# Performance work log

Hardware: AMD Instinct MI355X
Metric: run time of the kernel (lower is better)

## Reference

```python
import jax, jax.numpy as jnp
import numpy as np

T, B, H, O = 512, 64, 512, 128
G = 4 * H  # PyTorch gate order: i, f, g, o


def setup_inputs() -> dict:
    key = jax.random.key(0)
    ks = jax.random.split(key, 10)
    s = 1.0 / np.sqrt(H)
    return {
        "x": jax.random.normal(ks[0], (T, B, H), jnp.float32),
        "h0": jnp.zeros((1, B, H), jnp.float32),
        "c0": jnp.zeros((1, B, H), jnp.float32),
        "W_ih1": jax.random.normal(ks[1], (G, H), jnp.float32) * s,
        "W_hh1": jax.random.normal(ks[2], (G, H), jnp.float32) * s,
        "b_ih1": jax.random.normal(ks[3], (G,), jnp.float32) * s,
        "b_hh1": jax.random.normal(ks[4], (G,), jnp.float32) * s,
        "W_ih2": jax.random.normal(ks[5], (G, H), jnp.float32) * s,
        "W_hh2": jax.random.normal(ks[6], (G, H), jnp.float32) * s,
        "b_ih2": jax.random.normal(ks[7], (G,), jnp.float32) * s,
        "b_hh2": jax.random.normal(ks[8], (G,), jnp.float32) * s,
        "W_out": jax.random.normal(ks[9], (O, H), jnp.float32) * s,
        "b_out": jnp.zeros((O,), jnp.float32),
    }


def _lstm_layer(x, h0, c0, W_ih, W_hh, b_ih, b_hh):
    # x: [T,B,H]; h0,c0: [B,H]. PyTorch LSTM math, gate order i,f,g,o.
    xg = jnp.einsum('tbh,gh->tbg', x, W_ih) + b_ih + b_hh  # [T,B,4H]
    W_hh_T = W_hh.T

    def step(carry, xg_t):
        h, c = carry
        g = xg_t + h @ W_hh_T
        i, f, gc, o = jnp.split(g, 4, axis=-1)
        i = jax.nn.sigmoid(i)
        f = jax.nn.sigmoid(f)
        gc = jnp.tanh(gc)
        o = jax.nn.sigmoid(o)
        c = f * c + i * gc
        h = o * jnp.tanh(c)
        return (h, c), h

    (hT, cT), ys = jax.lax.scan(step, (h0, c0), xg)
    return ys, hT, cT


def reference(x, h0, c0, W_ih1, W_hh1, b_ih1, b_hh1, W_ih2, W_hh2, b_ih2, b_hh2, W_out, b_out):
    y1, h1, c1 = _lstm_layer(x, h0[0], c0[0], W_ih1, W_hh1, b_ih1, b_hh1)
    # Faithful quirk: lstm2 is initialized with lstm1's FINAL (h, c).
    y2, h2, c2 = _lstm_layer(y1, h1, c1, W_ih2, W_hh2, b_ih2, b_hh2)
    out = y2[-1] @ W_out.T + b_out  # Linear on last timestep; LogSoftmax is unused in forward
    return out, h2[None], c2[None]
```

## Files before the change

kernel.cpp:

```cpp
#include <hip/hip_runtime.h>

typedef unsigned short u16;
typedef unsigned int u32;
typedef unsigned long long u64;
using f32x4 = __attribute__((ext_vector_type(4))) float;
using s16x8 = __attribute__((ext_vector_type(8))) short;
using u64x2 = __attribute__((ext_vector_type(2))) unsigned long long;

constexpr int Tn = 512, Bn = 64, Hn = 512, Gn = 2048, On = 128;
constexpr int NS = 16;
constexpr int NG = 4;

constexpr size_t OFF_CMID = 0;
constexpr size_t OFF_HMID = OFF_CMID + (size_t)Bn * Hn * 4;
constexpr size_t OFF_XBF  = OFF_HMID + (size_t)Bn * Hn * 4;
constexpr size_t OFF_HT1  = OFF_XBF + (size_t)Tn * Bn * Hn * 2;
constexpr size_t OFF_HT2  = OFF_HT1 + (size_t)(Tn + 1) * Bn * Hn * 2;

__device__ __forceinline__ u16 f2b(float f) {
  union { float f; unsigned u; } v; v.f = f;
  unsigned r = v.u + 0x7fffu + ((v.u >> 16) & 1u);
  return (u16)(r >> 16);
}
__device__ __forceinline__ float b2f(u16 u) {
  union { unsigned u; float f; } v; v.u = ((unsigned)u) << 16; return v.f;
}
__device__ __forceinline__ s16x8 pack8(float4 lo, float4 hi) {
  s16x8 r;
  r[0] = (short)f2b(lo.x); r[1] = (short)f2b(lo.y); r[2] = (short)f2b(lo.z); r[3] = (short)f2b(lo.w);
  r[4] = (short)f2b(hi.x); r[5] = (short)f2b(hi.y); r[6] = (short)f2b(hi.z); r[7] = (short)f2b(hi.w);
  return r;
}
__device__ __forceinline__ float sigm(float x) {
  float e = __builtin_amdgcn_exp2f(-1.4426950408889634f * x);
  return __builtin_amdgcn_rcpf(1.0f + e);
}
__device__ __forceinline__ float tanh_(float x) {
  float e = __builtin_amdgcn_exp2f(-2.885390081777927f * x);
  return __builtin_amdgcn_rcpf(1.0f + e) * 2.0f - 1.0f;
}
__device__ __forceinline__ u64 ld64_sc(const u64* p) {
  return __hip_atomic_load(p, __ATOMIC_RELAXED, __HIP_MEMORY_SCOPE_AGENT);
}
__device__ __forceinline__ void st64_sc(u64* p, u64 v) {
  __hip_atomic_store(p, v, __ATOMIC_RELAXED, __HIP_MEMORY_SCOPE_AGENT);
}

__global__ __launch_bounds__(256)
void cvt_kernel(const float* __restrict__ in, u16* __restrict__ out, int n4) {
  const int i = blockIdx.x * 256 + threadIdx.x;
  if (i < n4) {
    float4 v = ((const float4*)in)[i];
    ushort4 o; o.x = f2b(v.x); o.y = f2b(v.y); o.z = f2b(v.z); o.w = f2b(v.w);
    ((ushort4*)out)[i] = o;
  }
}

__global__ __launch_bounds__(256, 1)
void scan_fused(const u16* __restrict__ xin, const float* __restrict__ Whh,
                const float* __restrict__ Wih, const float* __restrict__ bih,
                const float* __restrict__ bhh,
                const float* __restrict__ hinit, const float* __restrict__ cinit,
                u16* __restrict__ ht, float* __restrict__ h_fin, float* __restrict__ c_fin)
{
  const int g = blockIdx.x >> 4, s = blockIdx.x & (NS - 1);
  const int tid = threadIdx.x;
  const int lane = tid & 63, w = tid >> 6;
  const int x16 = lane & 15, grp = lane >> 4;
  const int jj = x16 & 7;
  const int j0 = s * 32 + w * 8;
  const int brow = g * 16;
  const int bth = brow + grp * 4;

  __shared__ char hlds[16 * 1024];
  __shared__ char xlds[2 * 16 * 1024];
  __shared__ u16 hstage[16][32];

  const size_t grow0 = (size_t)(0 * 2 + (x16 >> 3)) * Hn + j0 + jj;
  const size_t grow1 = (size_t)(2 + (x16 >> 3)) * Hn + j0 + jj;
  s16x8 bwh[2][16], bwi[2][16];
#pragma unroll
  for (int nt = 0; nt < 2; ++nt) {
    const size_t grow = nt ? grow1 : grow0;
#pragma unroll
    for (int ks = 0; ks < 16; ++ks) {
      const float* wp = Whh + grow * Hn + ks * 32 + grp * 8;
      float4 lo = *(const float4*)wp, hi = *(const float4*)(wp + 4);
      bwh[nt][ks] = pack8(lo, hi);
      const float* wq = Wih + grow * Hn + ks * 32 + grp * 8;
      float4 lo2 = *(const float4*)wq, hi2 = *(const float4*)(wq + 4);
      bwi[nt][ks] = pack8(lo2, hi2);
    }
  }
  const float bias0 = bih[grow0] + bhh[grow0];
  const float bias1 = bih[grow1] + bhh[grow1];

  float c[4];
#pragma unroll
  for (int r = 0; r < 4; ++r) c[r] = cinit[(size_t)(bth + r) * Hn + j0 + jj];

  if (tid < 128) {
    const int row = tid >> 3, cq = tid & 7;
    const float* hp = hinit + (size_t)(brow + row) * Hn + s * 32 + cq * 4;
    u64 v = (u64)f2b(hp[0]) | ((u64)f2b(hp[1]) << 16)
          | ((u64)f2b(hp[2]) << 32) | ((u64)f2b(hp[3]) << 48);
    st64_sc((u64*)(ht + (size_t)(brow + row) * Hn + s * 32 + cq * 4), v);
  }

  {
    const int row = tid >> 6, ci = tid & 63;
#pragma unroll
    for (int i = 0; i < 4; ++i) {
      const int rr = row + 4 * i;
      u64x2 q = *(const u64x2*)(xin + (size_t)(brow + rr) * Hn + ci * 8);
      *(u64x2*)(xlds + rr * 1024 + ((ci ^ (rr & 7)) * 16)) = q;
    }
  }
  __syncthreads();

  for (int t = 0; t < Tn; ++t) {
    const u16* rt = ht + (size_t)t * Bn * Hn;
    const u64* p0 = (const u64*)(rt + (size_t)(brow + (tid >> 6)) * Hn) + ((tid & 63) << 1);
    u64 v[8];
#pragma unroll
    for (int i = 0; i < 4; ++i) {
      v[2 * i]     = ld64_sc(p0 + i * 512);
      v[2 * i + 1] = ld64_sc(p0 + i * 512 + 1);
    }
    f32x4 acc0, acc1;
    acc0[0] = bias0; acc0[1] = bias0; acc0[2] = bias0; acc0[3] = bias0;
    acc1[0] = bias1; acc1[1] = bias1; acc1[2] = bias1; acc1[3] = bias1;
    {
      const char* xb = xlds + (size_t)(t & 1) * 16384;
#pragma unroll
      for (int ks = 0; ks < 16; ++ks) {
        const s16x8 a = *(const s16x8*)(xb + x16 * 1024 + ((((ks << 2) + grp) ^ jj) * 16));
        acc0 = __builtin_amdgcn_mfma_f32_16x16x32_bf16(a, bwi[0][ks], acc0, 0, 0, 0);
        acc1 = __builtin_amdgcn_mfma_f32_16x16x32_bf16(a, bwi[1][ks], acc1, 0, 0, 0);
      }
    }
    while (true) {
      bool all = true;
#pragma unroll
      for (int i = 0; i < 8; ++i) all = all && (v[i] != ~0ull);
      if (all) break;
      __builtin_amdgcn_s_sleep(1);
#pragma unroll
      for (int i = 0; i < 4; ++i) {
        if (v[2 * i]     == ~0ull) v[2 * i]     = ld64_sc(p0 + i * 512);
        if (v[2 * i + 1] == ~0ull) v[2 * i + 1] = ld64_sc(p0 + i * 512 + 1);
      }
    }
    {
      const int row = tid >> 6, ci = tid & 63;
#pragma unroll
      for (int i = 0; i < 4; ++i) {
        const int rr = row + 4 * i;
        u64x2 q; q[0] = v[2 * i]; q[1] = v[2 * i + 1];
        *(u64x2*)(hlds + rr * 1024 + ((ci ^ (rr & 7)) * 16)) = q;
      }
    }
    __syncthreads();
#pragma unroll
    for (int ks = 0; ks < 16; ++ks) {
      const s16x8 a = *(const s16x8*)(hlds + x16 * 1024 + ((((ks << 2) + grp) ^ jj) * 16));
      acc0 = __builtin_amdgcn_mfma_f32_16x16x32_bf16(a, bwh[0][ks], acc0, 0, 0, 0);
      acc1 = __builtin_amdgcn_mfma_f32_16x16x32_bf16(a, bwh[1][ks], acc1, 0, 0, 0);
    }
    float hv[4];
#pragma unroll
    for (int r = 0; r < 4; ++r) {
      const float p0v = acc0[r], p1v = acc1[r];
      const float q0 = __shfl_xor(p0v, 8, 64);
      const float q1 = __shfl_xor(p1v, 8, 64);
      const bool lo = (x16 < 8);
      const float gi = lo ? p0v : q0;
      const float gf = lo ? q0 : p0v;
      const float gg = lo ? p1v : q1;
      const float go = lo ? q1 : p1v;
      const float cn = sigm(gf) * c[r] + sigm(gi) * tanh_(gg);
      c[r] = cn;
      hv[r] = sigm(go) * tanh_(cn);
    }
    if (t == Tn - 1 && x16 < 8) {
#pragma unroll
      for (int r = 0; r < 4; ++r) {
        h_fin[(size_t)(bth + r) * Hn + j0 + jj] = hv[r];
        c_fin[(size_t)(bth + r) * Hn + j0 + jj] = c[r];
      }
    }
    {
      float a0 = hv[0], a1 = hv[1], a2 = hv[2], a3 = hv[3];
      const int p = x16 & 3;
      float tvu;
      tvu = (p & 1) ? a0 : a1;  tvu = __shfl_xor(tvu, 1, 64);
      if (p & 1) a0 = tvu; else a1 = tvu;
      tvu = (p & 1) ? a2 : a3;  tvu = __shfl_xor(tvu, 1, 64);
      if (p & 1) a2 = tvu; else a3 = tvu;
      tvu = (p & 2) ? a0 : a2;  tvu = __shfl_xor(tvu, 2, 64);
      if (p & 2) a0 = tvu; else a2 = tvu;
      tvu = (p & 2) ? a1 : a3;  tvu = __shfl_xor(tvu, 2, 64);
      if (p & 2) a1 = tvu; else a3 = tvu;
      if (x16 < 8) {
        const int cc = (x16 >> 2) & 1;
        const u64 yv = (u64)f2b(a0) | ((u64)f2b(a1) << 16)
                     | ((u64)f2b(a2) << 32) | ((u64)f2b(a3) << 48);
        *(u64*)&hstage[grp * 4 + p][w * 8 + cc * 4] = yv;
      }
    }
    __syncthreads();
    const int tn = (t + 1 < Tn) ? t + 1 : t;
    u64x2 xr[4];
    {
      const int row = tid >> 6, ci = tid & 63;
      const u16* xsrc = xin + (size_t)tn * Bn * Hn;
#pragma unroll
      for (int i = 0; i < 4; ++i)
        xr[i] = *(const u64x2*)(xsrc + (size_t)(brow + (row + 4 * i)) * Hn + ci * 8);
    }
    if (!(tid & 1)) {
      const int q = tid >> 1, row = q >> 3, cq = q & 7;
      const u64 yv = *(const u64*)&hstage[row][cq * 4];
      st64_sc((u64*)(ht + (size_t)(t + 1) * Bn * Hn + (size_t)(brow + row) * Hn + s * 32 + cq * 4), yv);
    }
    {
      const int row = tid >> 6, ci = tid & 63;
      char* xb = xlds + (size_t)((t + 1) & 1) * 16384;
#pragma unroll
      for (int i = 0; i < 4; ++i) {
        const int rr = row + 4 * i;
        *(u64x2*)(xb + rr * 1024 + ((ci ^ (rr & 7)) * 16)) = xr[i];
      }
    }
    __syncthreads();
  }
}

__global__ __launch_bounds__(128)
void out_kernel(const float* __restrict__ h2, const float* __restrict__ Wout,
                const float* __restrict__ bout, float* __restrict__ out)
{
  const int b = blockIdx.x, o = threadIdx.x;
  const float4* hp = (const float4*)(h2 + (size_t)b * Hn);
  const float4* wp = (const float4*)(Wout + (size_t)o * Hn);
  float acc = 0.f;
#pragma unroll 4
  for (int k = 0; k < Hn / 4; ++k) {
    float4 h4 = hp[k], w4 = wp[k];
    acc += h4.x * w4.x + h4.y * w4.y + h4.z * w4.z + h4.w * w4.w;
  }
  out[(size_t)b * On + o] = acc + bout[o];
}

extern "C" void kernel_launch(void* const* d_in, const int* in_sizes, int n_in,
                              void* d_out, int out_size, void* d_ws, size_t ws_size,
                              hipStream_t stream) {
  const float* x     = (const float*)d_in[0];
  const float* h0    = (const float*)d_in[1];
  const float* c0    = (const float*)d_in[2];
  const float* W_ih1 = (const float*)d_in[3];
  const float* W_hh1 = (const float*)d_in[4];
  const float* b_ih1 = (const float*)d_in[5];
  const float* b_hh1 = (const float*)d_in[6];
  const float* W_ih2 = (const float*)d_in[7];
  const float* W_hh2 = (const float*)d_in[8];
  const float* b_ih2 = (const float*)d_in[9];
  const float* b_hh2 = (const float*)d_in[10];
  const float* W_out = (const float*)d_in[11];
  const float* b_out = (const float*)d_in[12];

  float* out    = (float*)d_out;
  float* h2_out = out + (size_t)Bn * On;
  float* c2_out = h2_out + (size_t)Bn * Hn;

  char* w = (char*)d_ws;
  float* c_mid = (float*)(w + OFF_CMID);
  float* h_mid = (float*)(w + OFF_HMID);
  u16*   x_bf  = (u16*)(w + OFF_XBF);
  u16*   ht1   = (u16*)(w + OFF_HT1);
  u16*   ht2   = (u16*)(w + OFF_HT2);

  const size_t ht_bytes = (size_t)(Tn + 1) * Bn * Hn * 2;
  const int nx4 = Tn * Bn * Hn / 4;

  hipMemsetAsync(ht1, 0xFF, 2 * ht_bytes, stream);
  cvt_kernel<<<(nx4 + 255) / 256, 256, 0, stream>>>(x, x_bf, nx4);
  scan_fused<<<NG * NS, 256, 0, stream>>>(x_bf, W_hh1, W_ih1, b_ih1, b_hh1,
                                          h0, c0, ht1, h_mid, c_mid);
  scan_fused<<<NG * NS, 256, 0, stream>>>(ht1 + (size_t)Bn * Hn, W_hh2, W_ih2, b_ih2, b_hh2,
                                          h_mid, c_mid, ht2, h2_out, c2_out);
  out_kernel<<<Bn, 128, 0, stream>>>(h2_out, W_out, b_out, out);
}
```

Baseline: 2.968 ms.

## Hoist input projections into concurrent GEMM blocks overlapping the recurrent scan

The per-step input-projection MFMAs move out of the recurrent scan loop into separate GEMM workgroups that run in the same launch as the layer-1 scan. Those workgroups write a bf16 gate-preactivation buffer, and the scan polls it using a 0xFF sentinel. Layer-2's projection also runs concurrently, polling layer-1's h outputs, so layer 2's scan only does the recurrent matmul. This shortens the serial critical path per timestep. The cost is a much larger workspace, extra memsets, spin-wait polling, and reuse of the xg1 region as ht2 after the first kernel finishes. A fallback path runs when the workspace is too small.

```diff
diff --git a/kernel.cpp b/kernel.cpp
--- a/kernel.cpp
+++ b/kernel.cpp
@@ -5,17 +5,21 @@
 typedef unsigned long long u64;
 using f32x4 = __attribute__((ext_vector_type(4))) float;
 using s16x8 = __attribute__((ext_vector_type(8))) short;
+using u32x4 = __attribute__((ext_vector_type(4))) unsigned int;
 using u64x2 = __attribute__((ext_vector_type(2))) unsigned long long;
 
 constexpr int Tn = 512, Bn = 64, Hn = 512, Gn = 2048, On = 128;
 constexpr int NS = 16;
 constexpr int NG = 4;
 
+constexpr size_t HT_BYTES = (size_t)(Tn + 1) * Bn * Hn * 2;
+constexpr size_t XG_BYTES = (size_t)Tn * (size_t)Gn * Bn * 2;
 constexpr size_t OFF_CMID = 0;
 constexpr size_t OFF_HMID = OFF_CMID + (size_t)Bn * Hn * 4;
-constexpr size_t OFF_XBF  = OFF_HMID + (size_t)Bn * Hn * 4;
-constexpr size_t OFF_HT1  = OFF_XBF + (size_t)Tn * Bn * Hn * 2;
-constexpr size_t OFF_HT2  = OFF_HT1 + (size_t)(Tn + 1) * Bn * Hn * 2;
+constexpr size_t OFF_HT1  = OFF_HMID + (size_t)Bn * Hn * 4;
+constexpr size_t OFF_XG1  = OFF_HT1 + HT_BYTES;
+constexpr size_t OFF_XG2  = OFF_XG1 + XG_BYTES;
+constexpr size_t NEED_A   = OFF_XG2 + XG_BYTES;
 
 __device__ __forceinline__ u16 f2b(float f) {
   union { float f; unsigned u; } v; v.f = f;
@@ -45,25 +49,97 @@
 __device__ __forceinline__ void st64_sc(u64* p, u64 v) {
   __hip_atomic_store(p, v, __ATOMIC_RELAXED, __HIP_MEMORY_SCOPE_AGENT);
 }
-
-__global__ __launch_bounds__(256)
-void cvt_kernel(const float* __restrict__ in, u16* __restrict__ out, int n4) {
-  const int i = blockIdx.x * 256 + threadIdx.x;
-  if (i < n4) {
-    float4 v = ((const float4*)in)[i];
-    ushort4 o; o.x = f2b(v.x); o.y = f2b(v.y); o.z = f2b(v.z); o.w = f2b(v.w);
-    ((ushort4*)out)[i] = o;
-  }
-}
-
-__global__ __launch_bounds__(256, 1)
-void scan_fused(const u16* __restrict__ xin, const float* __restrict__ Whh,
-                const float* __restrict__ Wih, const float* __restrict__ bih,
-                const float* __restrict__ bhh,
-                const float* __restrict__ hinit, const float* __restrict__ cinit,
-                u16* __restrict__ ht, float* __restrict__ h_fin, float* __restrict__ c_fin)
-{
-  const int g = blockIdx.x >> 4, s = blockIdx.x & (NS - 1);
+__device__ __forceinline__ ushort4 u64_to_us4(u64 q) { union { u64 q; ushort4 v; } u; u.q = q; return u.v; }
+__device__ __forceinline__ s16x8 u32x4_to_s16x8(u32x4 a) { union { u32x4 a; s16x8 v; } u; u.a = a; return u.v; }
+
+template<bool AF32, bool POLLA>
+__device__ __forceinline__ void proj_core(
+    const int wg, const int nwg, const void* __restrict__ Ap,
+    const float* __restrict__ W, const float* __restrict__ bih,
+    const float* __restrict__ bhh, u16* __restrict__ xg)
+{
+  const int lane = threadIdx.x & 63, wave = threadIdx.x >> 6;
+  const int lrow = lane & 15, lk8 = (lane >> 4) << 3;
+  for (int tile = wg; tile < 4096; tile += nwg) {
+    const int m0 = (tile >> 4) * 128 + (wave & 1) * 64;
+    const int n0 = (tile & 15) * 128 + (wave >> 1) * 64;
+    f32x4 acc[4][4] = {};
+    for (int ks = 0; ks < 16; ++ks) {
+      const int k0 = ks * 32 + lk8;
+      s16x8 af[4], bfr[4];
+      if constexpr (AF32) {
+#pragma unroll
+        for (int mt = 0; mt < 4; ++mt) {
+          const float* ap = (const float*)Ap + (size_t)(m0 + mt * 16 + lrow) * Hn + k0;
+          float4 lo = *(const float4*)ap, hi = *(const float4*)(ap + 4);
+          af[mt] = pack8(lo, hi);
+        }
+      } else {
+        u32x4 a4[4];
+        const char* pa0 = (const char*)((const u16*)Ap + (size_t)(m0 + 0 * 16 + lrow) * Hn + k0);
+        const char* pa1 = (const char*)((const u16*)Ap + (size_t)(m0 + 1 * 16 + lrow) * Hn + k0);
+        const char* pa2 = (const char*)((const u16*)Ap + (size_t)(m0 + 2 * 16 + lrow) * Hn + k0);
+        const char* pa3 = (const char*)((const u16*)Ap + (size_t)(m0 + 3 * 16 + lrow) * Hn + k0);
+        asm volatile("global_load_dwordx4 %0, %1, off sc1" : "=v"(a4[0]) : "v"(pa0) : "memory");
+        asm volatile("global_load_dwordx4 %0, %1, off sc1" : "=v"(a4[1]) : "v"(pa1) : "memory");
+        asm volatile("global_load_dwordx4 %0, %1, off sc1" : "=v"(a4[2]) : "v"(pa2) : "memory");
+        asm volatile("global_load_dwordx4 %0, %1, off sc1" : "=v"(a4[3]) : "v"(pa3) : "memory");
+        asm volatile("s_waitcnt vmcnt(0)" ::: "memory");
+        while (true) {
+          bool bad = false;
+#pragma unroll
+          for (int mt = 0; mt < 4; ++mt)
+#pragma unroll
+            for (int d = 0; d < 4; ++d) bad = bad | (a4[mt][d] == 0xFFFFFFFFu);
+          if (!bad) break;
+          __builtin_amdgcn_s_sleep(1);
+          asm volatile("global_load_dwordx4 %0, %1, off sc1" : "=v"(a4[0]) : "v"(pa0) : "memory");
+          asm volatile("global_load_dwordx4 %0, %1, off sc1" : "=v"(a4[1]) : "v"(pa1) : "memory");
+          asm volatile("global_load_dwordx4 %0, %1, off sc1" : "=v"(a4[2]) : "v"(pa2) : "memory");
+          asm volatile("global_load_dwordx4 %0, %1, off sc1" : "=v"(a4[3]) : "v"(pa3) : "memory");
+          asm volatile("s_waitcnt vmcnt(0)" ::: "memory");
+        }
+#pragma unroll
+        for (int mt = 0; mt < 4; ++mt) af[mt] = u32x4_to_s16x8(a4[mt]);
+      }
+#pragma unroll
+      for (int nt = 0; nt < 4; ++nt) {
+        const float* wp = W + (size_t)(n0 + nt * 16 + lrow) * Hn + k0;
+        float4 lo = *(const float4*)wp, hi = *(const float4*)(wp + 4);
+        bfr[nt] = pack8(lo, hi);
+      }
+#pragma unroll
+      for (int mt = 0; mt < 4; ++mt)
+#pragma unroll
+        for (int nt = 0; nt < 4; ++nt)
+          acc[mt][nt] = __builtin_amdgcn_mfma_f32_16x16x32_bf16(af[mt], bfr[nt], acc[mt][nt], 0, 0, 0);
+    }
+    const int rbase = (lane >> 4) << 2;
+#pragma unroll
+    for (int nt = 0; nt < 4; ++nt) {
+      const int n = n0 + nt * 16 + lrow;
+      const float bias = bih[n] + bhh[n];
+#pragma unroll
+      for (int mt = 0; mt < 4; ++mt) {
+        const int m = m0 + mt * 16 + rbase;
+        const int t = m >> 6, b = m & 63;
+        const u64 pv = (u64)f2b(acc[mt][nt][0] + bias)
+                     | ((u64)f2b(acc[mt][nt][1] + bias) << 16)
+                     | ((u64)f2b(acc[mt][nt][2] + bias) << 32)
+                     | ((u64)f2b(acc[mt][nt][3] + bias) << 48);
+        st64_sc((u64*)(xg + ((size_t)t * Gn + n) * Bn + b), pv);
+      }
+    }
+  }
+}
+
+template<bool POLL_XG>
+__device__ __forceinline__ void scan_core(
+    const int wgid, const u16* __restrict__ xg, const float* __restrict__ Whh,
+    const float* __restrict__ hinit, const float* __restrict__ cinit,
+    u16* __restrict__ ht, float* __restrict__ h_fin, float* __restrict__ c_fin)
+{
+  const int g = wgid >> 4, s = wgid & (NS - 1);
   const int tid = threadIdx.x;
   const int lane = tid & 63, w = tid >> 6;
   const int x16 = lane & 15, grp = lane >> 4;
@@ -73,12 +149,11 @@
   const int bth = brow + grp * 4;
 
   __shared__ char hlds[16 * 1024];
-  __shared__ char xlds[2 * 16 * 1024];
   __shared__ u16 hstage[16][32];
 
-  const size_t grow0 = (size_t)(0 * 2 + (x16 >> 3)) * Hn + j0 + jj;
+  const size_t grow0 = (size_t)(x16 >> 3) * Hn + j0 + jj;
   const size_t grow1 = (size_t)(2 + (x16 >> 3)) * Hn + j0 + jj;
-  s16x8 bwh[2][16], bwi[2][16];
+  s16x8 bwh[2][16];
 #pragma unroll
   for (int nt = 0; nt < 2; ++nt) {
     const size_t grow = nt ? grow1 : grow0;
@@ -87,13 +162,8 @@
       const float* wp = Whh + grow * Hn + ks * 32 + grp * 8;
       float4 lo = *(const float4*)wp, hi = *(const float4*)(wp + 4);
       bwh[nt][ks] = pack8(lo, hi);
-      const float* wq = Wih + grow * Hn + ks * 32 + grp * 8;
-      float4 lo2 = *(const float4*)wq, hi2 = *(const float4*)(wq + 4);
-      bwi[nt][ks] = pack8(lo2, hi2);
-    }
-  }
-  const float bias0 = bih[grow0] + bhh[grow0];
-  const float bias1 = bih[grow1] + bhh[grow1];
+    }
+  }
 
   float c[4];
 #pragma unroll
@@ -107,16 +177,22 @@
     st64_sc((u64*)(ht + (size_t)(brow + row) * Hn + s * 32 + cq * 4), v);
   }
 
+  ushort4 xv0, xv1;
   {
-    const int row = tid >> 6, ci = tid & 63;
-#pragma unroll
-    for (int i = 0; i < 4; ++i) {
-      const int rr = row + 4 * i;
-      u64x2 q = *(const u64x2*)(xin + (size_t)(brow + rr) * Hn + ci * 8);
-      *(u64x2*)(xlds + rr * 1024 + ((ci ^ (rr & 7)) * 16)) = q;
-    }
-  }
-  __syncthreads();
+    const u16* xa = xg + grow0 * Bn + bth;
+    const u16* xb = xg + grow1 * Bn + bth;
+    if constexpr (POLL_XG) {
+      u64 a = ld64_sc((const u64*)xa), b = ld64_sc((const u64*)xb);
+      while (a == ~0ull || b == ~0ull) {
+        __builtin_amdgcn_s_sleep(2);
+        if (a == ~0ull) a = ld64_sc((const u64*)xa);
+        if (b == ~0ull) b = ld64_sc((const u64*)xb);
+      }
+      xv0 = u64_to_us4(a); xv1 = u64_to_us4(b);
+    } else {
+      xv0 = *(const ushort4*)xa; xv1 = *(const ushort4*)xb;
+    }
+  }
 
   for (int t = 0; t < Tn; ++t) {
     const u16* rt = ht + (size_t)t * Bn * Hn;
@@ -127,18 +203,6 @@
       v[2 * i]     = ld64_sc(p0 + i * 512);
       v[2 * i + 1] = ld64_sc(p0 + i * 512 + 1);
     }
-    f32x4 acc0, acc1;
-    acc0[0] = bias0; acc0[1] = bias0; acc0[2] = bias0; acc0[3] = bias0;
-    acc1[0] = bias1; acc1[1] = bias1; acc1[2] = bias1; acc1[3] = bias1;
-    {
-      const char* xb = xlds + (size_t)(t & 1) * 16384;
-#pragma unroll
-      for (int ks = 0; ks < 16; ++ks) {
-        const s16x8 a = *(const s16x8*)(xb + x16 * 1024 + ((((ks << 2) + grp) ^ jj) * 16));
-        acc0 = __builtin_amdgcn_mfma_f32_16x16x32_bf16(a, bwi[0][ks], acc0, 0, 0, 0);
-        acc1 = __builtin_amdgcn_mfma_f32_16x16x32_bf16(a, bwi[1][ks], acc1, 0, 0, 0);
-      }
-    }
     while (true) {
       bool all = true;
 #pragma unroll
@@ -161,6 +225,9 @@
       }
     }
     __syncthreads();
+    f32x4 acc0, acc1;
+    acc0[0] = b2f(xv0.x); acc0[1] = b2f(xv0.y); acc0[2] = b2f(xv0.z); acc0[3] = b2f(xv0.w);
+    acc1[0] = b2f(xv1.x); acc1[1] = b2f(xv1.y); acc1[2] = b2f(xv1.z); acc1[3] = b2f(xv1.w);
 #pragma unroll
     for (int ks = 0; ks < 16; ++ks) {
       const s16x8 a = *(const s16x8*)(hlds + x16 * 1024 + ((((ks << 2) + grp) ^ jj) * 16));
@@ -209,11 +276,227 @@
       }
     }
     __syncthreads();
-    const int tn = (t + 1 < Tn) ? t + 1 : t;
+    if (!(tid & 1)) {
+      const int q = tid >> 1, row = q >> 3, cq = q & 7;
+      const u64 yv = *(const u64*)&hstage[row][cq * 4];
+      st64_sc((u64*)(ht + (size_t)(t + 1) * Bn * Hn + (size_t)(brow + row) * Hn + s * 32 + cq * 4), yv);
+    }
+    const int tn2 = (t + 1 < Tn) ? t + 1 : t;
+    {
+      const u16* xa = xg + ((size_t)tn2 * Gn + grow0) * Bn + bth;
+      const u16* xb = xg + ((size_t)tn2 * Gn + grow1) * Bn + bth;
+      if constexpr (POLL_XG) {
+        u64 a = ld64_sc((const u64*)xa), b = ld64_sc((const u64*)xb);
+        while (a == ~0ull || b == ~0ull) {
+          __builtin_amdgcn_s_sleep(2);
+          if (a == ~0ull) a = ld64_sc((const u64*)xa);
+          if (b == ~0ull) b = ld64_sc((const u64*)xb);
+        }
+        xv0 = u64_to_us4(a); xv1 = u64_to_us4(b);
+      } else {
+        xv0 = *(const ushort4*)xa; xv1 = *(const ushort4*)xb;
+      }
+    }
+    __syncthreads();
+  }
+}
+
+__global__ __launch_bounds__(256, 1)
+void mega_full(const float* __restrict__ x,
+               const float* __restrict__ Wih1, const float* __restrict__ bih1, const float* __restrict__ bhh1,
+               const float* __restrict__ Whh1, const float* __restrict__ h0, const float* __restrict__ c0,
+               u16* __restrict__ ht1, u16* __restrict__ xg1,
+               const float* __restrict__ Wih2, const float* __restrict__ bih2, const float* __restrict__ bhh2,
+               u16* __restrict__ xg2, float* __restrict__ h_mid, float* __restrict__ c_mid)
+{
+  const int bid = blockIdx.x;
+  if (bid < 64)
+    scan_core<true>(bid, xg1, Whh1, h0, c0, ht1, h_mid, c_mid);
+  else if (bid < 160)
+    proj_core<true, false>(bid - 64, 96, x, Wih1, bih1, bhh1, xg1);
+  else
+    proj_core<false, true>(bid - 160, 96, ht1 + (size_t)Bn * Hn, Wih2, bih2, bhh2, xg2);
+}
+
+__global__ __launch_bounds__(256, 1)
+void mega_half(const float* __restrict__ x,
+               const float* __restrict__ Wih1, const float* __restrict__ bih1, const float* __restrict__ bhh1,
+               const float* __restrict__ Whh1, const float* __restrict__ h0, const float* __restrict__ c0,
+               u16* __restrict__ ht1, u16* __restrict__ xg1,
+               float* __restrict__ h_mid, float* __restrict__ c_mid)
+{
+  const int bid = blockIdx.x;
+  if (bid < 64)
+    scan_core<true>(bid, xg1, Whh1, h0, c0, ht1, h_mid, c_mid);
+  else
+    proj_core<true, false>(bid - 64, 192, x, Wih1, bih1, bhh1, xg1);
+}
+
+__global__ __launch_bounds__(256, 1)
+void scan_plain(const u16* __restrict__ xg, const float* __restrict__ Whh,
+                const float* __restrict__ hinit, const float* __restrict__ cinit,
+                u16* __restrict__ ht, float* __restrict__ h_fin, float* __restrict__ c_fin)
+{
+  scan_core<false>(blockIdx.x, xg, Whh, hinit, cinit, ht, h_fin, c_fin);
+}
+
+__global__ __launch_bounds__(256, 1)
+void scan_fused(const u16* __restrict__ xin, const float* __restrict__ Whh,
+                const float* __restrict__ Wih, const float* __restrict__ bih,
+                const float* __restrict__ bhh,
+                const float* __restrict__ hinit, const float* __restrict__ cinit,
+                u16* __restrict__ ht, float* __restrict__ h_fin, float* __restrict__ c_fin)
+{
+  const int g = blockIdx.x >> 4, s = blockIdx.x & (NS - 1);
+  const int tid = threadIdx.x;
+  const int lane = tid & 63, w = tid >> 6;
+  const int x16 = lane & 15, grp = lane >> 4;
+  const int jj = x16 & 7;
+  const int j0 = s * 32 + w * 8;
+  const int brow = g * 16;
+  const int bth = brow + grp * 4;
+
+  __shared__ char hlds[16 * 1024];
+  __shared__ char xlds[2 * 16 * 1024];
+  __shared__ u16 hstage[16][32];
+
+  const size_t grow0 = (size_t)(x16 >> 3) * Hn + j0 + jj;
+  const size_t grow1 = (size_t)(2 + (x16 >> 3)) * Hn + j0 + jj;
+  s16x8 bwh[2][16], bwi[2][16];
+#pragma unroll
+  for (int nt = 0; nt < 2; ++nt) {
+    const size_t grow = nt ? grow1 : grow0;
+#pragma unroll
+    for (int ks = 0; ks < 16; ++ks) {
+      const float* wp = Whh + grow * Hn + ks * 32 + grp * 8;
+      float4 lo = *(const float4*)wp, hi = *(const float4*)(wp + 4);
+      bwh[nt][ks] = pack8(lo, hi);
+      const float* wq = Wih + grow * Hn + ks * 32 + grp * 8;
+      float4 lo2 = *(const float4*)wq, hi2 = *(const float4*)(wq + 4);
+      bwi[nt][ks] = pack8(lo2, hi2);
+    }
+  }
+  const float bias0 = bih[grow0] + bhh[grow0];
+  const float bias1 = bih[grow1] + bhh[grow1];
+
+  float c[4];
+#pragma unroll
+  for (int r = 0; r < 4; ++r) c[r] = cinit[(size_t)(bth + r) * Hn + j0 + jj];
+
+  if (tid < 128) {
+    const int row = tid >> 3, cq = tid & 7;
+    const float* hp = hinit + (size_t)(brow + row) * Hn + s * 32 + cq * 4;
+    u64 v = (u64)f2b(hp[0]) | ((u64)f2b(hp[1]) << 16)
+          | ((u64)f2b(hp[2]) << 32) | ((u64)f2b(hp[3]) << 48);
+    st64_sc((u64*)(ht + (size_t)(brow + row) * Hn + s * 32 + cq * 4), v);
+  }
+  {
+    const int row = tid >> 6, ci = tid & 63;
+#pragma unroll
+    for (int i = 0; i < 4; ++i) {
+      const int rr = row + 4 * i;
+      u64x2 q = *(const u64x2*)(xin + (size_t)(brow + rr) * Hn + ci * 8);
+      *(u64x2*)(xlds + rr * 1024 + ((ci ^ (rr & 7)) * 16)) = q;
+    }
+  }
+  __syncthreads();
+
+  for (int t = 0; t < Tn; ++t) {
+    const u16* rt = ht + (size_t)t * Bn * Hn;
+    const u64* p0 = (const u64*)(rt + (size_t)(brow + (tid >> 6)) * Hn) + ((tid & 63) << 1);
+    u64 v[8];
+#pragma unroll
+    for (int i = 0; i < 4; ++i) {
+      v[2 * i]     = ld64_sc(p0 + i * 512);
+      v[2 * i + 1] = ld64_sc(p0 + i * 512 + 1);
+    }
+    f32x4 acc0, acc1;
+    acc0[0] = bias0; acc0[1] = bias0; acc0[2] = bias0; acc0[3] = bias0;
+    acc1[0] = bias1; acc1[1] = bias1; acc1[2] = bias1; acc1[3] = bias1;
+    {
+      const char* xb = xlds + (size_t)(t & 1) * 16384;
+#pragma unroll
+      for (int ks = 0; ks < 16; ++ks) {
+        const s16x8 a = *(const s16x8*)(xb + x16 * 1024 + ((((ks << 2) + grp) ^ jj) * 16));
+        acc0 = __builtin_amdgcn_mfma_f32_16x16x32_bf16(a, bwi[0][ks], acc0, 0, 0, 0);
+        acc1 = __builtin_amdgcn_mfma_f32_16x16x32_bf16(a, bwi[1][ks], acc1, 0, 0, 0);
+      }
+    }
+    while (true) {
+      bool all = true;
+#pragma unroll
+      for (int i = 0; i < 8; ++i) all = all && (v[i] != ~0ull);
+      if (all) break;
+      __builtin_amdgcn_s_sleep(1);
+#pragma unroll
+      for (int i = 0; i < 4; ++i) {
+        if (v[2 * i]     == ~0ull) v[2 * i]     = ld64_sc(p0 + i * 512);
+        if (v[2 * i + 1] == ~0ull) v[2 * i + 1] = ld64_sc(p0 + i * 512 + 1);
+      }
+    }
+    {
+      const int row = tid >> 6, ci = tid & 63;
+#pragma unroll
+      for (int i = 0; i < 4; ++i) {
+        const int rr = row + 4 * i;
+        u64x2 q; q[0] = v[2 * i]; q[1] = v[2 * i + 1];
+        *(u64x2*)(hlds + rr * 1024 + ((ci ^ (rr & 7)) * 16)) = q;
+      }
+    }
+    __syncthreads();
+#pragma unroll
+    for (int ks = 0; ks < 16; ++ks) {
+      const s16x8 a = *(const s16x8*)(hlds + x16 * 1024 + ((((ks << 2) + grp) ^ jj) * 16));
+      acc0 = __builtin_amdgcn_mfma_f32_16x16x32_bf16(a, bwh[0][ks], acc0, 0, 0, 0);
+      acc1 = __builtin_amdgcn_mfma_f32_16x16x32_bf16(a, bwh[1][ks], acc1, 0, 0, 0);
+    }
+    float hv[4];
+#pragma unroll
+    for (int r = 0; r < 4; ++r) {
+      const float p0v = acc0[r], p1v = acc1[r];
+      const float q0 = __shfl_xor(p0v, 8, 64);
+      const float q1 = __shfl_xor(p1v, 8, 64);
+      const bool lo = (x16 < 8);
+      const float gi = lo ? p0v : q0;
+      const float gf = lo ? q0 : p0v;
+      const float gg = lo ? p1v : q1;
+      const float go = lo ? q1 : p1v;
+      const float cn = sigm(gf) * c[r] + sigm(gi) * tanh_(gg);
+      c[r] = cn;
+      hv[r] = sigm(go) * tanh_(cn);
+    }
+    if (t == Tn - 1 && x16 < 8) {
+#pragma unroll
+      for (int r = 0; r < 4; ++r) {
+        h_fin[(size_t)(bth + r) * Hn + j0 + jj] = hv[r];
+        c_fin[(size_t)(bth + r) * Hn + j0 + jj] = c[r];
+      }
+    }
+    {
+      float a0 = hv[0], a1 = hv[1], a2 = hv[2], a3 = hv[3];
+      const int p = x16 & 3;
+      float tvu;
+      tvu = (p & 1) ? a0 : a1;  tvu = __shfl_xor(tvu, 1, 64);
+      if (p & 1) a0 = tvu; else a1 = tvu;
+      tvu = (p & 1) ? a2 : a3;  tvu = __shfl_xor(tvu, 1, 64);
+      if (p & 1) a2 = tvu; else a3 = tvu;
+      tvu = (p & 2) ? a0 : a2;  tvu = __shfl_xor(tvu, 2, 64);
+      if (p & 2) a0 = tvu; else a2 = tvu;
+      tvu = (p & 2) ? a1 : a3;  tvu = __shfl_xor(tvu, 2, 64);
+      if (p & 2) a1 = tvu; else a3 = tvu;
+      if (x16 < 8) {
+        const int cc = (x16 >> 2) & 1;
+        const u64 yv = (u64)f2b(a0) | ((u64)f2b(a1) << 16)
+                     | ((u64)f2b(a2) << 32) | ((u64)f2b(a3) << 48);
+        *(u64*)&hstage[grp * 4 + p][w * 8 + cc * 4] = yv;
+      }
+    }
+    __syncthreads();
+    const int tn2 = (t + 1 < Tn) ? t + 1 : t;
     u64x2 xr[4];
     {
       const int row = tid >> 6, ci = tid & 63;
-      const u16* xsrc = xin + (size_t)tn * Bn * Hn;
+      const u16* xsrc = xin + (size_t)tn2 * Bn * Hn;
 #pragma unroll
       for (int i = 0; i < 4; ++i)
         xr[i] = *(const u64x2*)(xsrc + (size_t)(brow + (row + 4 * i)) * Hn + ci * 8);
@@ -276,18 +559,25 @@
   char* w = (char*)d_ws;
   float* c_mid = (float*)(w + OFF_CMID);
   float* h_mid = (float*)(w + OFF_HMID);
-  u16*   x_bf  = (u16*)(w + OFF_XBF);
   u16*   ht1   = (u16*)(w + OFF_HT1);
-  u16*   ht2   = (u16*)(w + OFF_HT2);
-
-  const size_t ht_bytes = (size_t)(Tn + 1) * Bn * Hn * 2;
-  const int nx4 = Tn * Bn * Hn / 4;
-
-  hipMemsetAsync(ht1, 0xFF, 2 * ht_bytes, stream);
-  cvt_kernel<<<(nx4 + 255) / 256, 256, 0, stream>>>(x, x_bf, nx4);
-  scan_fused<<<NG * NS, 256, 0, stream>>>(x_bf, W_hh1, W_ih1, b_ih1, b_hh1,
-                                          h0, c0, ht1, h_mid, c_mid);
-  scan_fused<<<NG * NS, 256, 0, stream>>>(ht1 + (size_t)Bn * Hn, W_hh2, W_ih2, b_ih2, b_hh2,
-                                          h_mid, c_mid, ht2, h2_out, c2_out);
+  u16*   xg1   = (u16*)(w + OFF_XG1);
+  u16*   ht2   = (u16*)(w + OFF_XG1);
+  u16*   xg2   = (u16*)(w + OFF_XG2);
+
+  hipMemsetAsync(ht1, 0xFF, HT_BYTES, stream);
+  hipMemsetAsync(xg1, 0xFF, XG_BYTES, stream);
+
+  if (ws_size >= NEED_A) {
+    mega_full<<<256, 256, 0, stream>>>(x, W_ih1, b_ih1, b_hh1, W_hh1, h0, c0,
+                                       ht1, xg1, W_ih2, b_ih2, b_hh2, xg2, h_mid, c_mid);
+    hipMemsetAsync(ht2, 0xFF, HT_BYTES, stream);
+    scan_plain<<<NG * NS, 256, 0, stream>>>(xg2, W_hh2, h_mid, c_mid, ht2, h2_out, c2_out);
+  } else {
+    mega_half<<<256, 256, 0, stream>>>(x, W_ih1, b_ih1, b_hh1, W_hh1, h0, c0,
+                                       ht1, xg1, h_mid, c_mid);
+    hipMemsetAsync(ht2, 0xFF, HT_BYTES, stream);
+    scan_fused<<<NG * NS, 256, 0, stream>>>(ht1 + (size_t)Bn * Hn, W_hh2, W_ih2, b_ih2, b_hh2,
+                                            h_mid, c_mid, ht2, h2_out, c2_out);
+  }
   out_kernel<<<Bn, 128, 0, stream>>>(h2_out, W_out, b_out, out);
 }
```

Result: faster. 2.793 ms (-5.9%).

## Hoist input projections into concurrent GEMM blocks overlapped with layer-1 scan

Applied to the files above, without the earlier changes.

Moves the input-to-hidden projection out of the per-timestep recurrence into a separate tiled MFMA GEMM that writes bf16 gate pre-activations to a global buffer. A single large launch runs the layer-1 scan blocks next to blocks computing layer-1 and layer-2 projections. The layer-2 projection polls layer-1 hidden states as they appear, using 0xFF sentinel flags. Each serial step then only does the recurrent matmul plus a small gate load, which shortens the critical path. In exchange it relies on all 256 workgroups being co-resident, adds spin-polling traffic, and reuses one gate buffer for both layers, so correctness depends on the ordering of producers and consumers.

```diff
diff --git a/kernel.cpp b/kernel.cpp
--- a/kernel.cpp
+++ b/kernel.cpp
@@ -5,17 +5,19 @@
 typedef unsigned long long u64;
 using f32x4 = __attribute__((ext_vector_type(4))) float;
 using s16x8 = __attribute__((ext_vector_type(8))) short;
+using u32x4 = __attribute__((ext_vector_type(4))) unsigned int;
 using u64x2 = __attribute__((ext_vector_type(2))) unsigned long long;
 
 constexpr int Tn = 512, Bn = 64, Hn = 512, Gn = 2048, On = 128;
 constexpr int NS = 16;
 constexpr int NG = 4;
 
+constexpr size_t HT_BYTES = (size_t)(Tn + 1) * Bn * Hn * 2;
+constexpr size_t XG_BYTES = (size_t)Tn * (size_t)Gn * Bn * 2;
 constexpr size_t OFF_CMID = 0;
 constexpr size_t OFF_HMID = OFF_CMID + (size_t)Bn * Hn * 4;
-constexpr size_t OFF_XBF  = OFF_HMID + (size_t)Bn * Hn * 4;
-constexpr size_t OFF_HT1  = OFF_XBF + (size_t)Tn * Bn * Hn * 2;
-constexpr size_t OFF_HT2  = OFF_HT1 + (size_t)(Tn + 1) * Bn * Hn * 2;
+constexpr size_t OFF_HT1  = OFF_HMID + (size_t)Bn * Hn * 4;
+constexpr size_t OFF_XG   = OFF_HT1 + HT_BYTES;
 
 __device__ __forceinline__ u16 f2b(float f) {
   union { float f; unsigned u; } v; v.f = f;
@@ -45,25 +47,97 @@
 __device__ __forceinline__ void st64_sc(u64* p, u64 v) {
   __hip_atomic_store(p, v, __ATOMIC_RELAXED, __HIP_MEMORY_SCOPE_AGENT);
 }
-
-__global__ __launch_bounds__(256)
-void cvt_kernel(const float* __restrict__ in, u16* __restrict__ out, int n4) {
-  const int i = blockIdx.x * 256 + threadIdx.x;
-  if (i < n4) {
-    float4 v = ((const float4*)in)[i];
-    ushort4 o; o.x = f2b(v.x); o.y = f2b(v.y); o.z = f2b(v.z); o.w = f2b(v.w);
-    ((ushort4*)out)[i] = o;
-  }
-}
-
-__global__ __launch_bounds__(256, 1)
-void scan_fused(const u16* __restrict__ xin, const float* __restrict__ Whh,
-                const float* __restrict__ Wih, const float* __restrict__ bih,
-                const float* __restrict__ bhh,
-                const float* __restrict__ hinit, const float* __restrict__ cinit,
-                u16* __restrict__ ht, float* __restrict__ h_fin, float* __restrict__ c_fin)
-{
-  const int g = blockIdx.x >> 4, s = blockIdx.x & (NS - 1);
+__device__ __forceinline__ ushort4 u64_to_us4(u64 q) { union { u64 q; ushort4 v; } u; u.q = q; return u.v; }
+__device__ __forceinline__ s16x8 u32x4_to_s16x8(u32x4 a) { union { u32x4 a; s16x8 v; } u; u.a = a; return u.v; }
+
+template<bool AF32, bool POLLA>
+__device__ __forceinline__ void proj_core(
+    const int wg, const int nwg, const void* __restrict__ Ap,
+    const float* __restrict__ W, const float* __restrict__ bih,
+    const float* __restrict__ bhh, u16* __restrict__ xg)
+{
+  const int lane = threadIdx.x & 63, wave = threadIdx.x >> 6;
+  const int lrow = lane & 15, lk8 = (lane >> 4) << 3;
+  for (int tile = wg; tile < 4096; tile += nwg) {
+    const int m0 = (tile >> 4) * 128 + (wave & 1) * 64;
+    const int n0 = (tile & 15) * 128 + (wave >> 1) * 64;
+    f32x4 acc[4][4] = {};
+    for (int ks = 0; ks < 16; ++ks) {
+      const int k0 = ks * 32 + lk8;
+      s16x8 af[4], bfr[4];
+      if constexpr (AF32) {
+#pragma unroll
+        for (int mt = 0; mt < 4; ++mt) {
+          const float* ap = (const float*)Ap + (size_t)(m0 + mt * 16 + lrow) * Hn + k0;
+          float4 lo = *(const float4*)ap, hi = *(const float4*)(ap + 4);
+          af[mt] = pack8(lo, hi);
+        }
+      } else {
+        u32x4 a4[4];
+        const char* pa0 = (const char*)((const u16*)Ap + (size_t)(m0 + 0 * 16 + lrow) * Hn + k0);
+        const char* pa1 = (const char*)((const u16*)Ap + (size_t)(m0 + 1 * 16 + lrow) * Hn + k0);
+        const char* pa2 = (const char*)((const u16*)Ap + (size_t)(m0 + 2 * 16 + lrow) * Hn + k0);
+        const char* pa3 = (const char*)((const u16*)Ap + (size_t)(m0 + 3 * 16 + lrow) * Hn + k0);
+        asm volatile("global_load_dwordx4 %0, %1, off sc1" : "=v"(a4[0]) : "v"(pa0) : "memory");
+        asm volatile("global_load_dwordx4 %0, %1, off sc1" : "=v"(a4[1]) : "v"(pa1) : "memory");
+        asm volatile("global_load_dwordx4 %0, %1, off sc1" : "=v"(a4[2]) : "v"(pa2) : "memory");
+        asm volatile("global_load_dwordx4 %0, %1, off sc1" : "=v"(a4[3]) : "v"(pa3) : "memory");
+        asm volatile("s_waitcnt vmcnt(0)" ::: "memory");
+        while (true) {
+          bool bad = false;
+#pragma unroll
+          for (int mt = 0; mt < 4; ++mt)
+#pragma unroll
+            for (int d = 0; d < 4; ++d) bad = bad | (a4[mt][d] == 0xFFFFFFFFu);
+          if (!bad) break;
+          __builtin_amdgcn_s_sleep(8);
+          asm volatile("global_load_dwordx4 %0, %1, off sc1" : "=v"(a4[0]) : "v"(pa0) : "memory");
+          asm volatile("global_load_dwordx4 %0, %1, off sc1" : "=v"(a4[1]) : "v"(pa1) : "memory");
+          asm volatile("global_load_dwordx4 %0, %1, off sc1" : "=v"(a4[2]) : "v"(pa2) : "memory");
+          asm volatile("global_load_dwordx4 %0, %1, off sc1" : "=v"(a4[3]) : "v"(pa3) : "memory");
+          asm volatile("s_waitcnt vmcnt(0)" ::: "memory");
+        }
+#pragma unroll
+        for (int mt = 0; mt < 4; ++mt) af[mt] = u32x4_to_s16x8(a4[mt]);
+      }
+#pragma unroll
+      for (int nt = 0; nt < 4; ++nt) {
+        const float* wp = W + (size_t)(n0 + nt * 16 + lrow) * Hn + k0;
+        float4 lo = *(const float4*)wp, hi = *(const float4*)(wp + 4);
+        bfr[nt] = pack8(lo, hi);
+      }
+#pragma unroll
+      for (int mt = 0; mt < 4; ++mt)
+#pragma unroll
+        for (int nt = 0; nt < 4; ++nt)
+          acc[mt][nt] = __builtin_amdgcn_mfma_f32_16x16x32_bf16(af[mt], bfr[nt], acc[mt][nt], 0, 0, 0);
+    }
+    const int rbase = (lane >> 4) << 2;
+#pragma unroll
+    for (int nt = 0; nt < 4; ++nt) {
+      const int n = n0 + nt * 16 + lrow;
+      const float bias = bih[n] + bhh[n];
+#pragma unroll
+      for (int mt = 0; mt < 4; ++mt) {
+        const int m = m0 + mt * 16 + rbase;
+        const int t = m >> 6, b = m & 63;
+        const u64 pv = (u64)f2b(acc[mt][nt][0] + bias)
+                     | ((u64)f2b(acc[mt][nt][1] + bias) << 16)
+                     | ((u64)f2b(acc[mt][nt][2] + bias) << 32)
+                     | ((u64)f2b(acc[mt][nt][3] + bias) << 48);
+        st64_sc((u64*)(xg + ((size_t)t * Gn + n) * Bn + b), pv);
+      }
+    }
+  }
+}
+
+template<bool POLL_XG>
+__device__ __forceinline__ void scan_core(
+    const int wgid, const u16* __restrict__ xg, const float* __restrict__ Whh,
+    const float* __restrict__ hinit, const float* __restrict__ cinit,
+    u16* __restrict__ ht, float* __restrict__ h_fin, float* __restrict__ c_fin)
+{
+  const int g = wgid >> 4, s = wgid & (NS - 1);
   const int tid = threadIdx.x;
   const int lane = tid & 63, w = tid >> 6;
   const int x16 = lane & 15, grp = lane >> 4;
@@ -73,12 +147,11 @@
   const int bth = brow + grp * 4;
 
   __shared__ char hlds[16 * 1024];
-  __shared__ char xlds[2 * 16 * 1024];
   __shared__ u16 hstage[16][32];
 
-  const size_t grow0 = (size_t)(0 * 2 + (x16 >> 3)) * Hn + j0 + jj;
+  const size_t grow0 = (size_t)(x16 >> 3) * Hn + j0 + jj;
   const size_t grow1 = (size_t)(2 + (x16 >> 3)) * Hn + j0 + jj;
-  s16x8 bwh[2][16], bwi[2][16];
+  s16x8 bwh[2][16];
 #pragma unroll
   for (int nt = 0; nt < 2; ++nt) {
     const size_t grow = nt ? grow1 : grow0;
@@ -87,13 +160,8 @@
       const float* wp = Whh + grow * Hn + ks * 32 + grp * 8;
       float4 lo = *(const float4*)wp, hi = *(const float4*)(wp + 4);
       bwh[nt][ks] = pack8(lo, hi);
-      const float* wq = Wih + grow * Hn + ks * 32 + grp * 8;
-      float4 lo2 = *(const float4*)wq, hi2 = *(const float4*)(wq + 4);
-      bwi[nt][ks] = pack8(lo2, hi2);
-    }
-  }
-  const float bias0 = bih[grow0] + bhh[grow0];
-  const float bias1 = bih[grow1] + bhh[grow1];
+    }
+  }
 
   float c[4];
 #pragma unroll
@@ -107,16 +175,22 @@
     st64_sc((u64*)(ht + (size_t)(brow + row) * Hn + s * 32 + cq * 4), v);
   }
 
+  ushort4 xv0, xv1;
   {
-    const int row = tid >> 6, ci = tid & 63;
-#pragma unroll
-    for (int i = 0; i < 4; ++i) {
-      const int rr = row + 4 * i;
-      u64x2 q = *(const u64x2*)(xin + (size_t)(brow + rr) * Hn + ci * 8);
-      *(u64x2*)(xlds + rr * 1024 + ((ci ^ (rr & 7)) * 16)) = q;
-    }
-  }
-  __syncthreads();
+    const u16* xa = xg + grow0 * Bn + bth;
+    const u16* xb = xg + grow1 * Bn + bth;
+    if constexpr (POLL_XG) {
+      u64 a = ld64_sc((const u64*)xa), b = ld64_sc((const u64*)xb);
+      while (a == ~0ull || b == ~0ull) {
+        __builtin_amdgcn_s_sleep(2);
+        if (a == ~0ull) a = ld64_sc((const u64*)xa);
+        if (b == ~0ull) b = ld64_sc((const u64*)xb);
+      }
+      xv0 = u64_to_us4(a); xv1 = u64_to_us4(b);
+    } else {
+      xv0 = *(const ushort4*)xa; xv1 = *(const ushort4*)xb;
+    }
+  }
 
   for (int t = 0; t < Tn; ++t) {
     const u16* rt = ht + (size_t)t * Bn * Hn;
@@ -127,18 +201,6 @@
       v[2 * i]     = ld64_sc(p0 + i * 512);
       v[2 * i + 1] = ld64_sc(p0 + i * 512 + 1);
     }
-    f32x4 acc0, acc1;
-    acc0[0] = bias0; acc0[1] = bias0; acc0[2] = bias0; acc0[3] = bias0;
-    acc1[0] = bias1; acc1[1] = bias1; acc1[2] = bias1; acc1[3] = bias1;
-    {
-      const char* xb = xlds + (size_t)(t & 1) * 16384;
-#pragma unroll
-      for (int ks = 0; ks < 16; ++ks) {
-        const s16x8 a = *(const s16x8*)(xb + x16 * 1024 + ((((ks << 2) + grp) ^ jj) * 16));
-        acc0 = __builtin_amdgcn_mfma_f32_16x16x32_bf16(a, bwi[0][ks], acc0, 0, 0, 0);
-        acc1 = __builtin_amdgcn_mfma_f32_16x16x32_bf16(a, bwi[1][ks], acc1, 0, 0, 0);
-      }
-    }
     while (true) {
       bool all = true;
 #pragma unroll
@@ -161,6 +223,9 @@
       }
     }
     __syncthreads();
+    f32x4 acc0, acc1;
+    acc0[0] = b2f(xv0.x); acc0[1] = b2f(xv0.y); acc0[2] = b2f(xv0.z); acc0[3] = b2f(xv0.w);
+    acc1[0] = b2f(xv1.x); acc1[1] = b2f(xv1.y); acc1[2] = b2f(xv1.z); acc1[3] = b2f(xv1.w);
 #pragma unroll
     for (int ks = 0; ks < 16; ++ks) {
       const s16x8 a = *(const s16x8*)(hlds + x16 * 1024 + ((((ks << 2) + grp) ^ jj) * 16));
@@ -209,31 +274,54 @@
       }
     }
     __syncthreads();
-    const int tn = (t + 1 < Tn) ? t + 1 : t;
-    u64x2 xr[4];
-    {
-      const int row = tid >> 6, ci = tid & 63;
-      const u16* xsrc = xin + (size_t)tn * Bn * Hn;
-#pragma unroll
-      for (int i = 0; i < 4; ++i)
-        xr[i] = *(const u64x2*)(xsrc + (size_t)(brow + (row + 4 * i)) * Hn + ci * 8);
-    }
     if (!(tid & 1)) {
       const int q = tid >> 1, row = q >> 3, cq = q & 7;
       const u64 yv = *(const u64*)&hstage[row][cq * 4];
       st64_sc((u64*)(ht + (size_t)(t + 1) * Bn * Hn + (size_t)(brow + row) * Hn + s * 32 + cq * 4), yv);
     }
+    const int tn2 = (t + 1 < Tn) ? t + 1 : t;
     {
-      const int row = tid >> 6, ci = tid & 63;
-      char* xb = xlds + (size_t)((t + 1) & 1) * 16384;
-#pragma unroll
-      for (int i = 0; i < 4; ++i) {
-        const int rr = row + 4 * i;
-        *(u64x2*)(xb + rr * 1024 + ((ci ^ (rr & 7)) * 16)) = xr[i];
+      const u16* xa = xg + ((size_t)tn2 * Gn + grow0) * Bn + bth;
+      const u16* xb = xg + ((size_t)tn2 * Gn + grow1) * Bn + bth;
+      if constexpr (POLL_XG) {
+        u64 a = ld64_sc((const u64*)xa), b = ld64_sc((const u64*)xb);
+        while (a == ~0ull || b == ~0ull) {
+          __builtin_amdgcn_s_sleep(2);
+          if (a == ~0ull) a = ld64_sc((const u64*)xa);
+          if (b == ~0ull) b = ld64_sc((const u64*)xb);
+        }
+        xv0 = u64_to_us4(a); xv1 = u64_to_us4(b);
+      } else {
+        xv0 = *(const ushort4*)xa; xv1 = *(const ushort4*)xb;
       }
     }
     __syncthreads();
   }
+}
+
+__global__ __launch_bounds__(256, 1)
+void mega_full(const float* __restrict__ x,
+               const float* __restrict__ Wih1, const float* __restrict__ bih1, const float* __restrict__ bhh1,
+               const float* __restrict__ Whh1, const float* __restrict__ h0, const float* __restrict__ c0,
+               u16* __restrict__ ht1, u16* __restrict__ xg,
+               const float* __restrict__ Wih2, const float* __restrict__ bih2, const float* __restrict__ bhh2,
+               float* __restrict__ h_mid, float* __restrict__ c_mid)
+{
+  const int bid = blockIdx.x;
+  if (bid < 64)
+    scan_core<true>(bid, xg, Whh1, h0, c0, ht1, h_mid, c_mid);
+  else if (bid < 160)
+    proj_core<true, false>(bid - 64, 96, x, Wih1, bih1, bhh1, xg);
+  else
+    proj_core<false, true>(bid - 160, 96, ht1 + (size_t)Bn * Hn, Wih2, bih2, bhh2, xg);
+}
+
+__global__ __launch_bounds__(256, 1)
+void scan_plain(const u16* __restrict__ xg, const float* __restrict__ Whh,
+                const float* __restrict__ hinit, const float* __restrict__ cinit,
+                u16* __restrict__ ht, float* __restrict__ h_fin, float* __restrict__ c_fin)
+{
+  scan_core<false>(blockIdx.x, xg, Whh, hinit, cinit, ht, h_fin, c_fin);
 }
 
 __global__ __launch_bounds__(128)
@@ -276,18 +364,15 @@
   char* w = (char*)d_ws;
   float* c_mid = (float*)(w + OFF_CMID);
   float* h_mid = (float*)(w + OFF_HMID);
-  u16*   x_bf  = (u16*)(w + OFF_XBF);
   u16*   ht1   = (u16*)(w + OFF_HT1);
-  u16*   ht2   = (u16*)(w + OFF_HT2);
-
-  const size_t ht_bytes = (size_t)(Tn + 1) * Bn * Hn * 2;
-  const int nx4 = Tn * Bn * Hn / 4;
-
-  hipMemsetAsync(ht1, 0xFF, 2 * ht_bytes, stream);
-  cvt_kernel<<<(nx4 + 255) / 256, 256, 0, stream>>>(x, x_bf, nx4);
-  scan_fused<<<NG * NS, 256, 0, stream>>>(x_bf, W_hh1, W_ih1, b_ih1, b_hh1,
-                                          h0, c0, ht1, h_mid, c_mid);
-  scan_fused<<<NG * NS, 256, 0, stream>>>(ht1 + (size_t)Bn * Hn, W_hh2, W_ih2, b_ih2, b_hh2,
-                                          h_mid, c_mid, ht2, h2_out, c2_out);
+  u16*   xg    = (u16*)(w + OFF_XG);
+
+  hipMemsetAsync(ht1, 0xFF, HT_BYTES, stream);
+  hipMemsetAsync(xg, 0xFF, XG_BYTES, stream);
+
+  mega_full<<<256, 256, 0, stream>>>(x, W_ih1, b_ih1, b_hh1, W_hh1, h0, c0,
+                                     ht1, xg, W_ih2, b_ih2, b_hh2, h_mid, c_mid);
+  hipMemsetAsync(ht1, 0xFF, HT_BYTES, stream);
+  scan_plain<<<NG * NS, 256, 0, stream>>>(xg, W_hh2, h_mid, c_mid, ht1, h2_out, c2_out);
   out_kernel<<<Bn, 128, 0, stream>>>(h2_out, W_out, b_out, out);
 }
```

Measured after the change: 2.642 ms. 1.12x faster.
